# Kernel tuning notes

Hardware: AMD Instinct MI355X
Metric: run time of the kernel (lower is better)

The kernel has to match this reference:

```python
import jax, jax.numpy as jnp
import numpy as np

D = 1024       # num_feature == heads*dim_head
NHEADS = 16
HD = 64
INNER = NHEADS * HD
FF = 2048      # hardcoded mlp_dim in CSGO_model
L = 4          # depth
NOUT = 26      # hardcoded number of InvDynamic heads
IDH = 512      # inverse_dynamic_dim
B = 64
T = 32         # horizon


def _ln(x, g=None, b=None, eps=1e-5):
    mu = jnp.mean(x, axis=-1, keepdims=True)
    var = jnp.mean((x - mu) ** 2, axis=-1, keepdims=True)
    y = (x - mu) * jax.lax.rsqrt(var + eps)
    if g is not None:
        y = y * g + b
    return y


def setup_inputs() -> dict:
    key = jax.random.key(0)
    ks = jax.random.split(key, 20)
    s = 0.02
    inp = {
        'x': jax.random.normal(ks[0], (B, T, D), jnp.float32),
        # transformer params, stacked over depth L
        'qkv_w': jax.random.normal(ks[1], (L, D, 3 * INNER), jnp.float32) * s,
        'out_w': jax.random.normal(ks[2], (L, INNER, D), jnp.float32) * s,
        'out_b': jnp.zeros((L, D), jnp.float32),
        'attn_ln_g': jnp.ones((L, D), jnp.float32),
        'attn_ln_b': jnp.zeros((L, D), jnp.float32),
        'ff_ln_g': jnp.ones((L, D), jnp.float32),
        'ff_ln_b': jnp.zeros((L, D), jnp.float32),
        'ff_w1': jax.random.normal(ks[3], (L, D, FF), jnp.float32) * s,
        'ff_b1': jnp.zeros((L, FF), jnp.float32),
        'ff_w2': jax.random.normal(ks[4], (L, FF, D), jnp.float32) * s,
        'ff_b2': jnp.zeros((L, D), jnp.float32),
        # 26 InvDynamic heads, stacked
        'head_w1': jax.random.normal(ks[5], (NOUT, 2 * D, IDH), jnp.float32) * s,
        'head_b1': jnp.zeros((NOUT, IDH), jnp.float32),
        'head_w2': jax.random.normal(ks[6], (NOUT, IDH, IDH), jnp.float32) * s,
        'head_b2': jnp.zeros((NOUT, IDH), jnp.float32),
        'head_w3': jax.random.normal(ks[7], (NOUT, IDH, 1), jnp.float32) * s,
        'head_b3': jnp.zeros((NOUT, 1), jnp.float32),
    }
    return inp


def _forward(x, qkv_w, out_w, out_b, attn_ln_g, attn_ln_b, ff_ln_g, ff_ln_b,
             ff_w1, ff_b1, ff_w2, ff_b2,
             head_w1, head_b1, head_w2, head_b2, head_w3, head_b3):
    scale = HD ** -0.5

    def block(h, p):
        (qw, ow, ob, ag, ab, fg, fb, w1, b1, w2, b2) = p
        # x = attn(prenorm_ln(mid_ln(x))) + x  (mid LayerNorm has no affine, eps=1e-6)
        y = _ln(h, eps=1e-6)
        y = _ln(y, ag, ab)
        qkv = y @ qw                               # [B,T,3*INNER]
        q, k, v = jnp.split(qkv, 3, axis=-1)
        def split_heads(t):
            return t.reshape(t.shape[0], t.shape[1], NHEADS, HD).transpose(0, 2, 1, 3)
        q, k, v = split_heads(q), split_heads(k), split_heads(v)
        attn = jax.nn.softmax(jnp.einsum('bhqd,bhkd->bhqk', q, k) * scale, axis=-1)
        o = jnp.einsum('bhqk,bhkd->bhqd', attn, v)
        o = o.transpose(0, 2, 1, 3).reshape(h.shape[0], h.shape[1], INNER)
        h = h + (o @ ow + ob)
        # x = ff(prenorm_ln(x)) + x
        y = _ln(h, fg, fb)
        y = jax.nn.gelu(y @ w1 + b1, approximate=False) @ w2 + b2
        return h + y, None

    params = (qkv_w, out_w, out_b, attn_ln_g, attn_ln_b, ff_ln_g, ff_ln_b,
              ff_w1, ff_b1, ff_w2, ff_b2)
    x, _ = jax.lax.scan(block, x, params)

    # x_comb = concat(x[:,0], x[:,1])  -> [B, 2D]
    x_comb = jnp.concatenate([x[:, 0, :], x[:, 1, :]], axis=1)
    # 26 independent 3-layer MLP heads, batched as grouped GEMMs
    h1 = jax.nn.relu(jnp.einsum('bd,ndk->bnk', x_comb, head_w1) + head_b1)
    h2 = jax.nn.relu(jnp.einsum('bnk,nkj->bnj', h1, head_w2) + head_b2)
    out = jnp.einsum('bnk,nkj->bnj', h2, head_w3) + head_b3   # [B,26,1]
    return out


def reference(x, qkv_w, out_w, out_b, attn_ln_g, attn_ln_b, ff_ln_g, ff_ln_b,
              ff_w1, ff_b1, ff_w2, ff_b2,
              head_w1, head_b1, head_w2, head_b2, head_w3, head_b3):
    return _forward(x, qkv_w, out_w, out_b, attn_ln_g, attn_ln_b, ff_ln_g,
                    ff_ln_b, ff_w1, ff_b1, ff_w2, ff_b2,
                    head_w1, head_b1, head_w2, head_b2, head_w3, head_b3)
```

## Files before the change

### kernel.cpp

```cpp
#include <hip/hip_runtime.h>
#include <math.h>

static constexpr int BATCH = 64;
static constexpr int SEQ   = 32;
static constexpr int TOK   = BATCH * SEQ;
static constexpr int DIM   = 1024;
static constexpr int NH    = 16;
static constexpr int HDIM  = 64;
static constexpr int FFD   = 2048;
static constexpr int LAYERS= 4;
static constexpr int NHEAD_OUT = 26;
static constexpr int IDH   = 512;

typedef __bf16 bf16_t;
typedef __bf16 bf16x4 __attribute__((ext_vector_type(4)));
typedef __bf16 bf16x8 __attribute__((ext_vector_type(8)));
typedef float  f32x4  __attribute__((ext_vector_type(4)));
typedef float  f32x16 __attribute__((ext_vector_type(16)));
typedef unsigned short us4 __attribute__((ext_vector_type(4)));
typedef unsigned short us8 __attribute__((ext_vector_type(8)));

__device__ __forceinline__ unsigned short f2bfu(float f) {
    return __builtin_bit_cast(unsigned short, (bf16_t)f);
}

__device__ __forceinline__ void gload_lds16(const void* gp, void* lp) {
    __builtin_amdgcn_global_load_lds(
        (const __attribute__((address_space(1))) unsigned int*)gp,
        (__attribute__((address_space(3))) unsigned int*)lp,
        16, 0, 0);
}

__device__ __forceinline__ float block_sum(float v, float* red) {
    #pragma unroll
    for (int off = 32; off > 0; off >>= 1) v += __shfl_down(v, off);
    int lane = threadIdx.x & 63;
    int w    = threadIdx.x >> 6;
    if (lane == 0) red[w] = v;
    __syncthreads();
    float t = red[0] + red[1] + red[2] + red[3];
    __syncthreads();
    return t;
}

template<bool PRE, bool F32IN>
__global__ __launch_bounds__(256) void ln_kernel(const void* __restrict__ xv,
                                                 const float* __restrict__ g,
                                                 const float* __restrict__ b,
                                                 bf16_t* __restrict__ y,
                                                 bf16_t* __restrict__ hout) {
    __shared__ float red[4];
    long row = blockIdx.x;
    int tid = threadIdx.x;
    float4 v;
    if (F32IN) {
        const float* xr = (const float*)xv + row * DIM;
        v = *(const float4*)(xr + tid * 4);
        us4 hc;
        hc.x = f2bfu(v.x); hc.y = f2bfu(v.y); hc.z = f2bfu(v.z); hc.w = f2bfu(v.w);
        *(us4*)(hout + row * DIM + tid * 4) = hc;
        v.x = (float)(bf16_t)v.x; v.y = (float)(bf16_t)v.y;
        v.z = (float)(bf16_t)v.z; v.w = (float)(bf16_t)v.w;
    } else {
        const bf16_t* xr = (const bf16_t*)xv + row * DIM;
        bf16x4 r4 = *(const bf16x4*)(xr + tid * 4);
        v.x = (float)r4[0]; v.y = (float)r4[1]; v.z = (float)r4[2]; v.w = (float)r4[3];
    }
    if (PRE) {
        float s  = block_sum(v.x + v.y + v.z + v.w, red);
        float mu = s * (1.0f / DIM);
        v.x -= mu; v.y -= mu; v.z -= mu; v.w -= mu;
        float ss = block_sum(v.x*v.x + v.y*v.y + v.z*v.z + v.w*v.w, red);
        float r  = 1.0f / sqrtf(ss * (1.0f / DIM) + 1e-6f);
        v.x *= r; v.y *= r; v.z *= r; v.w *= r;
    }
    float s  = block_sum(v.x + v.y + v.z + v.w, red);
    float mu = s * (1.0f / DIM);
    v.x -= mu; v.y -= mu; v.z -= mu; v.w -= mu;
    float ss = block_sum(v.x*v.x + v.y*v.y + v.z*v.z + v.w*v.w, red);
    float r  = 1.0f / sqrtf(ss * (1.0f / DIM) + 1e-5f);
    float4 gg = *(const float4*)(g + tid * 4);
    float4 bb = *(const float4*)(b + tid * 4);
    us4 o;
    o.x = f2bfu(v.x * r * gg.x + bb.x);
    o.y = f2bfu(v.y * r * gg.y + bb.y);
    o.z = f2bfu(v.z * r * gg.z + bb.z);
    o.w = f2bfu(v.w * r * gg.w + bb.w);
    *(us4*)(y + row * DIM + tid * 4) = o;
}

struct TxPack {
    const float* src[4];
    bf16_t*      dst[4];
    int K[4], N[4];
    int blk0[4];
};

__global__ __launch_bounds__(256) void txd(TxPack p) {
    int bid = blockIdx.x;
    int s = 0;
    #pragma unroll
    for (int i = 1; i < 4; ++i) if (bid >= p.blk0[i]) s = i;
    int base = (bid - p.blk0[s]) * 4;
    int K = p.K[s], N = p.N[s];
    int nkb = K >> 6;
    int cpg = (N >> 5) * nkb;
    int kk = threadIdx.x >> 6;
    int l  = threadIdx.x & 63;
    int nl = l & 31, k8 = (l >> 5) * 8;
    #pragma unroll
    for (int qq = 0; qq < 2; ++qq) {
        int c0 = base + qq * 2, c1 = c0 + 1;
        int g0 = c0 / cpg, r0 = c0 - g0 * cpg;
        int g1 = c1 / cpg, r1 = c1 - g1 * cpg;
        int ns0 = r0 / nkb, kt0 = r0 - ns0 * nkb;
        int ns1 = r1 / nkb, kt1 = r1 - ns1 * nkb;
        const float* s0 = p.src[s] + (long)g0 * K * N
                        + (long)(kt0 * 64 + kk * 16 + k8) * N + ns0 * 32 + nl;
        const float* s1 = p.src[s] + (long)g1 * K * N
                        + (long)(kt1 * 64 + kk * 16 + k8) * N + ns1 * 32 + nl;
        float av[8], bv[8];
        #pragma unroll
        for (int j = 0; j < 8; ++j) av[j] = s0[(long)j * N];
        #pragma unroll
        for (int j = 0; j < 8; ++j) bv[j] = s1[(long)j * N];
        us8 oa, ob2;
        #pragma unroll
        for (int j = 0; j < 8; ++j) { oa[j] = f2bfu(av[j]); ob2[j] = f2bfu(bv[j]); }
        *(us8*)(p.dst[s] + (long)c0 * 2048 + kk * 512 + l * 8) = oa;
        *(us8*)(p.dst[s] + (long)c1 * 2048 + kk * 512 + l * 8) = ob2;
    }
}

template<int BM, int BN, int WM, int WN, int EPI>
__global__ __launch_bounds__(256) void gemm32(
    const bf16_t* __restrict__ A, const bf16_t* __restrict__ BT,
    const float* __restrict__ bias, const bf16_t* __restrict__ resid,
    bf16_t* __restrict__ Ch,
    int M, int N, int K)
{
    constexpr int WAVES_N = BN / WN;
    constexpr int FM = WM / 32, FN = WN / 32;
    constexpr int NSTG = BM / 32 + BN / 32;

    __shared__ bf16_t As[2][BM * 64];
    __shared__ bf16_t Bs[2][BN * 64];

    int tid  = threadIdx.x;
    int wave = tid >> 6, lane = tid & 63;
    int wr = wave / WAVES_N, wc = wave % WAVES_N;
    int m0 = blockIdx.y * BM, n0 = blockIdx.x * BN;

    f32x16 acc[FM][FN];
    #pragma unroll
    for (int m = 0; m < FM; ++m)
        #pragma unroll
        for (int n = 0; n < FN; ++n)
            #pragma unroll
            for (int r = 0; r < 16; ++r)
                acc[m][n][r] = 0.f;

    long rsb = (long)K * 2;
    int  lr  = lane & 31;
    int  lkb = (lane >> 5) * 16;
    int  nkb = K >> 6;

    const char* Abase = (const char*)A + (long)(m0 + lr) * rsb + lkb;
    const char* Bbase = (const char*)BT + (long)(n0 >> 5) * nkb * 4096 + lane * 16;

    auto stage = [&](int c, int t) {
        long kb = (long)t * 128;
        #pragma unroll
        for (int i = 0; i < BM / 32; ++i) {
            int b = i * 4 + wave;
            gload_lds16(Abase + (long)(b >> 2) * 32 * rsb + (b & 3) * 32 + kb,
                        (char*)&As[c][0] + b * 1024);
        }
        #pragma unroll
        for (int i = 0; i < BN / 32; ++i) {
            int b = i * 4 + wave;
            gload_lds16(Bbase + ((long)(b >> 2) * nkb + t) * 4096 + (b & 3) * 1024,
                        (char*)&Bs[c][0] + b * 1024);
        }
    };

    int nt = K >> 6;
    stage(0, 0);
    int cur = 0;
    for (int t = 0; t < nt; ++t) {
        if (t + 1 < nt) {
            stage(cur ^ 1, t + 1);
            asm volatile("s_waitcnt vmcnt(%c0)" :: "i"(NSTG) : "memory");
        } else {
            asm volatile("s_waitcnt vmcnt(0)" ::: "memory");
        }
        __builtin_amdgcn_s_barrier();
        asm volatile("" ::: "memory");
        bf16x8 af[FM][4], bq[FN][4];
        #pragma unroll
        for (int m = 0; m < FM; ++m)
            #pragma unroll
            for (int kk = 0; kk < 4; ++kk)
                af[m][kk] = *(const bf16x8*)((const char*)&As[cur][0] +
                            ((wr * FM + m) * 4 + kk) * 1024 + (lane << 4));
        #pragma unroll
        for (int n = 0; n < FN; ++n)
            #pragma unroll
            for (int kk = 0; kk < 4; ++kk)
                bq[n][kk] = *(const bf16x8*)((const char*)&Bs[cur][0] +
                            ((wc * FN + n) * 4 + kk) * 1024 + (lane << 4));
        #pragma unroll
        for (int kk = 0; kk < 4; ++kk)
            #pragma unroll
            for (int m = 0; m < FM; ++m)
                #pragma unroll
                for (int n = 0; n < FN; ++n)
                    acc[m][n] = __builtin_amdgcn_mfma_f32_32x32x16_bf16(
                        af[m][kk], bq[n][kk], acc[m][n], 0, 0, 0);
        asm volatile("" ::: "memory");
        __builtin_amdgcn_s_barrier();
        cur ^= 1;
    }

    int rbase = 4 * (lane >> 5);
    #pragma unroll
    for (int m = 0; m < FM; ++m) {
        #pragma unroll
        for (int n = 0; n < FN; ++n) {
            int colI = n0 + wc * WN + n * 32 + (lane & 31);
            float bb = (EPI != 0) ? bias[colI] : 0.f;
            #pragma unroll
            for (int r = 0; r < 16; ++r) {
                int rowI = m0 + wr * WM + m * 32 + rbase + (r & 3) + 8 * (r >> 2);
                float v = acc[m][n][r] + bb;
                if (EPI == 2) v = 0.5f * v * (1.0f + erff(v * 0.70710678118654752f));
                long off = (long)rowI * N + colI;
                if (EPI == 1) v += (float)resid[off];
                Ch[off] = (bf16_t)v;
            }
        }
    }
}

__global__ __launch_bounds__(256) void gemm_hd(
    const bf16_t* __restrict__ A, const float* __restrict__ Bw,
    const float* __restrict__ bias, bf16_t* __restrict__ C,
    int N, int K, long aStride, long sA, long sB, long sbias, long sC)
{
    long g = blockIdx.z;
    A += g * sA;
    const float* Bp = Bw + g * sB;
    bias += g * sbias;
    bf16_t* Cp = C + g * sC;

    __shared__ bf16_t As[2][64 * 64];
    __shared__ float  Bf[2][64 * 64];

    int tid = threadIdx.x, wave = tid >> 6, lane = tid & 63;
    int wr = wave >> 1, wc = wave & 1;
    int n0 = blockIdx.x * 64;

    f32x4 acc[2][2];
    #pragma unroll
    for (int m = 0; m < 2; ++m)
        #pragma unroll
        for (int n = 0; n < 2; ++n)
            acc[m][n] = f32x4{0.f, 0.f, 0.f, 0.f};

    long rsb = aStride * 2;
    int  lr  = lane & 15;
    int  lkb = (lane >> 4) * 16;
    const char* Abase = (const char*)A + (long)lr * rsb + lkb;

    auto stage = [&](int c, int t) {
        long kb = (long)t * 128;
        #pragma unroll
        for (int i = 0; i < 2; ++i) {
            int b = i * 4 + wave;
            gload_lds16(Abase + (long)(b >> 1) * 16 * rsb + (b & 1) * 64 + kb,
                        (char*)&As[c][0] + b * 1024);
        }
        #pragma unroll
        for (int i = 0; i < 4; ++i) {
            int ch = i * 4 + wave;
            int row = ch * 4 + (lane >> 4);
            gload_lds16((const char*)Bp + ((long)(t * 64 + row) * N + n0) * 4 + (lane & 15) * 16,
                        (char*)&Bf[c][0] + ch * 1024);
        }
    };

    int nt = K >> 6;
    stage(0, 0);
    int cur = 0;
    for (int t = 0; t < nt; ++t) {
        if (t + 1 < nt) {
            stage(cur ^ 1, t + 1);
            asm volatile("s_waitcnt vmcnt(6)" ::: "memory");
        } else {
            asm volatile("s_waitcnt vmcnt(0)" ::: "memory");
        }
        __builtin_amdgcn_s_barrier();
        asm volatile("" ::: "memory");
        bf16x8 af[2][2], bq[2][2];
        #pragma unroll
        for (int m = 0; m < 2; ++m)
            #pragma unroll
            for (int h = 0; h < 2; ++h)
                af[m][h] = *(const bf16x8*)((const char*)&As[cur][0] +
                           ((wr * 2 + m) * 2 + h) * 1024 + (lane << 4));
        #pragma unroll
        for (int n = 0; n < 2; ++n) {
            int nl = wc * 32 + n * 16 + lr;
            #pragma unroll
            for (int h = 0; h < 2; ++h) {
                #pragma unroll
                for (int j = 0; j < 8; ++j) {
                    float v = Bf[cur][(h * 32 + (lane >> 4) * 8 + j) * 64 + nl];
                    bq[n][h][j] = (bf16_t)v;
                }
            }
        }
        #pragma unroll
        for (int h = 0; h < 2; ++h)
            #pragma unroll
            for (int m = 0; m < 2; ++m)
                #pragma unroll
                for (int n = 0; n < 2; ++n)
                    acc[m][n] = __builtin_amdgcn_mfma_f32_16x16x32_bf16(
                        af[m][h], bq[n][h], acc[m][n], 0, 0, 0);
        asm volatile("" ::: "memory");
        __builtin_amdgcn_s_barrier();
        cur ^= 1;
    }

    int lq = (lane >> 4) * 4;
    #pragma unroll
    for (int m = 0; m < 2; ++m) {
        #pragma unroll
        for (int n = 0; n < 2; ++n) {
            int colI = n0 + wc * 32 + n * 16 + lr;
            float bb = bias[colI];
            #pragma unroll
            for (int j = 0; j < 4; ++j) {
                int rowI = wr * 32 + m * 16 + lq + j;
                float v = fmaxf(acc[m][n][j] + bb, 0.0f);
                Cp[(long)rowI * N + colI] = (bf16_t)v;
            }
        }
    }
}

__global__ __launch_bounds__(256) void attn_kernel(const bf16_t* __restrict__ qkv,
                                                   bf16_t* __restrict__ o) {
    int bh = blockIdx.x;
    int b  = bh >> 4;
    int hh = bh & 15;
    __shared__ float qs[32][65];
    __shared__ float kt[64][36];
    __shared__ float vs[32][68];
    __shared__ float ps[32][33];
    const bf16_t* base = qkv + (long)b * SEQ * (3 * DIM) + hh * HDIM;
    int tid = threadIdx.x;

    {
        int t = tid >> 3, c = (tid & 7) * 8;
        bf16x8 qv = *(const bf16x8*)(base + (long)t * 3 * DIM + c);
        bf16x8 kv = *(const bf16x8*)(base + (long)t * 3 * DIM + DIM + c);
        bf16x8 vv = *(const bf16x8*)(base + (long)t * 3 * DIM + 2 * DIM + c);
        #pragma unroll
        for (int j = 0; j < 8; ++j) {
            int d = c + j;
            qs[t][d] = (float)qv[j];
            kt[d][(((t >> 2) ^ ((d >> 2) & 7)) << 2) + (t & 3)] = (float)kv[j];
            vs[t][d] = (float)vv[j];
        }
    }
    __syncthreads();

    {
        int r  = tid >> 3;
        int c0 = (tid & 7) * 4;
        f32x4 acc = {0.f, 0.f, 0.f, 0.f};
        #pragma unroll
        for (int d = 0; d < 64; ++d) {
            float qv = qs[r][d];
            float4 kv = *(const float4*)&kt[d][(((c0 >> 2) ^ ((d >> 2) & 7)) << 2)];
            acc[0] = fmaf(qv, kv.x, acc[0]);
            acc[1] = fmaf(qv, kv.y, acc[1]);
            acc[2] = fmaf(qv, kv.z, acc[2]);
            acc[3] = fmaf(qv, kv.w, acc[3]);
        }
        #pragma unroll
        for (int i = 0; i < 4; ++i) ps[r][c0 + i] = acc[i] * 0.125f;
    }
    __syncthreads();

    if (tid < 32) {
        float mx = -1e30f;
        for (int c = 0; c < 32; ++c) mx = fmaxf(mx, ps[tid][c]);
        float sum = 0.f;
        for (int c = 0; c < 32; ++c) { float e = expf(ps[tid][c] - mx); ps[tid][c] = e; sum += e; }
        float inv = 1.f / sum;
        for (int c = 0; c < 32; ++c) ps[tid][c] *= inv;
    }
    __syncthreads();

    {
        int r  = tid >> 3;
        int d0 = (tid & 7) * 8;
        float acc[8] = {};
        #pragma unroll
        for (int c = 0; c < 32; ++c) {
            float pv = ps[r][c];
            float4 v0 = *(const float4*)&vs[c][d0];
            float4 v1 = *(const float4*)&vs[c][d0 + 4];
            acc[0] = fmaf(pv, v0.x, acc[0]);
            acc[1] = fmaf(pv, v0.y, acc[1]);
            acc[2] = fmaf(pv, v0.z, acc[2]);
            acc[3] = fmaf(pv, v0.w, acc[3]);
            acc[4] = fmaf(pv, v1.x, acc[4]);
            acc[5] = fmaf(pv, v1.y, acc[5]);
            acc[6] = fmaf(pv, v1.z, acc[6]);
            acc[7] = fmaf(pv, v1.w, acc[7]);
        }
        us8 ov;
        #pragma unroll
        for (int j = 0; j < 8; ++j) ov[j] = f2bfu(acc[j]);
        *(us8*)(o + (long)b * SEQ * DIM + (long)r * DIM + hh * HDIM + d0) = ov;
    }
}

__global__ __launch_bounds__(256) void head3_kernel(const bf16_t* __restrict__ h2,
                                                    const float* __restrict__ w3,
                                                    const float* __restrict__ b3,
                                                    float* __restrict__ out) {
    int gid  = blockIdx.x * 256 + threadIdx.x;
    int wave = gid >> 6;
    int lane = gid & 63;
    if (wave >= NHEAD_OUT * BATCH) return;
    int n = wave >> 6;
    int b = wave & 63;
    const bf16_t* a = h2 + ((long)n * BATCH + b) * IDH;
    const float*  w = w3 + (long)n * IDH;
    float acc = 0.f;
    #pragma unroll
    for (int i = lane; i < IDH; i += 64) acc = fmaf((float)a[i], w[i], acc);
    #pragma unroll
    for (int off = 32; off > 0; off >>= 1) acc += __shfl_down(acc, off);
    if (lane == 0) out[b * NHEAD_OUT + n] = acc + b3[n];
}

extern "C" void kernel_launch(void* const* d_in, const int* in_sizes, int n_in,
                              void* d_out, int out_size, void* d_ws, size_t ws_size,
                              hipStream_t stream) {
    const float* x      = (const float*)d_in[0];
    const float* qkv_w  = (const float*)d_in[1];
    const float* out_w  = (const float*)d_in[2];
    const float* out_b  = (const float*)d_in[3];
    const float* attn_g = (const float*)d_in[4];
    const float* attn_b = (const float*)d_in[5];
    const float* ff_g   = (const float*)d_in[6];
    const float* ff_b   = (const float*)d_in[7];
    const float* ff_w1  = (const float*)d_in[8];
    const float* ff_b1  = (const float*)d_in[9];
    const float* ff_w2  = (const float*)d_in[10];
    const float* ff_b2  = (const float*)d_in[11];
    const float* hw1    = (const float*)d_in[12];
    const float* hb1    = (const float*)d_in[13];
    const float* hw2    = (const float*)d_in[14];
    const float* hb2    = (const float*)d_in[15];
    const float* hw3    = (const float*)d_in[16];
    const float* hb3    = (const float*)d_in[17];
    float* out = (float*)d_out;

    char* p = (char*)d_ws;
    bf16_t* h     = (bf16_t*)p;           p += (long)TOK * DIM * 2;
    bf16_t* qkvb  = (bf16_t*)p;           p += (long)TOK * 3 * DIM * 2;
    bf16_t* y     = (bf16_t*)p;           p += (long)TOK * DIM * 2;
    bf16_t* ob    = (bf16_t*)p;           p += (long)TOK * DIM * 2;
    bf16_t* ffb   = (bf16_t*)p;           p += (long)TOK * FFD * 2;
    bf16_t* h1    = (bf16_t*)p;           p += (long)NHEAD_OUT * BATCH * IDH * 2;
    bf16_t* h2    = (bf16_t*)p;           p += (long)NHEAD_OUT * BATCH * IDH * 2;
    bf16_t* qkvwt = (bf16_t*)p;           p += (long)LAYERS * DIM * 3 * DIM * 2;
    bf16_t* outwt = (bf16_t*)p;           p += (long)LAYERS * DIM * DIM * 2;
    bf16_t* ff1t  = (bf16_t*)p;           p += (long)LAYERS * DIM * FFD * 2;
    bf16_t* ff2t  = (bf16_t*)p;           p += (long)LAYERS * FFD * DIM * 2;

    TxPack tp;
    tp.src[0] = qkv_w; tp.dst[0] = qkvwt; tp.K[0] = DIM; tp.N[0] = 3 * DIM;
    tp.src[1] = out_w; tp.dst[1] = outwt; tp.K[1] = DIM; tp.N[1] = DIM;
    tp.src[2] = ff_w1; tp.dst[2] = ff1t;  tp.K[2] = DIM; tp.N[2] = FFD;
    tp.src[3] = ff_w2; tp.dst[3] = ff2t;  tp.K[3] = FFD; tp.N[3] = DIM;
    int nblk = 0;
    for (int i = 0; i < 4; ++i) {
        tp.blk0[i] = nblk;
        nblk += LAYERS * (tp.N[i] >> 5) * (tp.K[i] >> 6) / 4;
    }
    txd<<<nblk, 256, 0, stream>>>(tp);

    for (int l = 0; l < LAYERS; ++l) {
        if (l == 0)
            ln_kernel<true, true><<<TOK, 256, 0, stream>>>(
                x, attn_g, attn_b, y, h);
        else
            ln_kernel<true, false><<<TOK, 256, 0, stream>>>(
                h, attn_g + l * DIM, attn_b + l * DIM, y, nullptr);
        gemm32<64, 128, 32, 64, 0><<<dim3(3 * DIM / 128, TOK / 64), 256, 0, stream>>>(
            y, qkvwt + (long)l * DIM * 3 * DIM, nullptr, nullptr, qkvb,
            TOK, 3 * DIM, DIM);
        attn_kernel<<<BATCH * NH, 256, 0, stream>>>(qkvb, ob);
        gemm32<64, 64, 32, 32, 1><<<dim3(DIM / 64, TOK / 64), 256, 0, stream>>>(
            ob, outwt + (long)l * DIM * DIM, out_b + l * DIM, h, h,
            TOK, DIM, DIM);
        ln_kernel<false, false><<<TOK, 256, 0, stream>>>(
            h, ff_g + l * DIM, ff_b + l * DIM, y, nullptr);
        gemm32<64, 128, 32, 64, 2><<<dim3(FFD / 128, TOK / 64), 256, 0, stream>>>(
            y, ff1t + (long)l * DIM * FFD, ff_b1 + l * FFD, nullptr, ffb,
            TOK, FFD, DIM);
        gemm32<64, 64, 32, 32, 1><<<dim3(DIM / 64, TOK / 64), 256, 0, stream>>>(
            ffb, ff2t + (long)l * FFD * DIM, ff_b2 + l * DIM, h, h,
            TOK, DIM, FFD);
    }

    gemm_hd<<<dim3(IDH / 64, 1, NHEAD_OUT), 256, 0, stream>>>(
        h, hw1, hb1, h1,
        IDH, 2 * DIM, (long)SEQ * DIM,
        0, (long)2 * DIM * IDH, IDH, (long)BATCH * IDH);
    gemm_hd<<<dim3(IDH / 64, 1, NHEAD_OUT), 256, 0, stream>>>(
        h1, hw2, hb2, h2,
        IDH, IDH, IDH,
        (long)BATCH * IDH, (long)IDH * IDH, IDH, (long)BATCH * IDH);
    head3_kernel<<<(NHEAD_OUT * BATCH * 64) / 256, 256, 0, stream>>>(h2, hw3, hb3, out);
}
```

Before: 526.5 us.

## Overlap next-layer weight conversion with current-layer GEMMs via extra blocks

```diff
diff --git a/kernel.cpp b/kernel.cpp
--- a/kernel.cpp
+++ b/kernel.cpp
@@ -29,6 +29,44 @@
         (const __attribute__((address_space(1))) unsigned int*)gp,
         (__attribute__((address_space(3))) unsigned int*)lp,
         16, 0, 0);
+}
+
+__device__ __forceinline__ void tx_chunks4(const float* __restrict__ src,
+                                           bf16_t* __restrict__ dst,
+                                           int K, int N, int base4) {
+    int nkb = K >> 6;
+    int kk = threadIdx.x >> 6;
+    int l  = threadIdx.x & 63;
+    int nl = l & 31, k8 = (l >> 5) * 8;
+    int base = base4 * 4;
+    #pragma unroll
+    for (int q = 0; q < 4; ++q) {
+        int chunk = base + q;
+        int ns = chunk / nkb;
+        int kt = chunk - ns * nkb;
+        int n = ns * 32 + nl;
+        int kb = kt * 64 + kk * 16 + k8;
+        us8 o;
+        #pragma unroll
+        for (int j = 0; j < 8; ++j)
+            o[j] = f2bfu(src[(long)(kb + j) * N + n]);
+        *(us8*)(dst + (long)chunk * 2048 + kk * 512 + l * 8) = o;
+    }
+}
+
+struct TxPack {
+    const float* src[4];
+    bf16_t*      dst[4];
+    int K[4], N[4];
+    int blk0[4];
+};
+
+__global__ __launch_bounds__(256) void txd(TxPack p) {
+    int bid = blockIdx.x;
+    int s = 0;
+    #pragma unroll
+    for (int i = 1; i < 4; ++i) if (bid >= p.blk0[i]) s = i;
+    tx_chunks4(p.src[s], p.dst[s], p.K[s], p.N[s], bid - p.blk0[s]);
 }
 
 __device__ __forceinline__ float block_sum(float v, float* red) {
@@ -89,55 +127,14 @@
     *(us4*)(y + row * DIM + tid * 4) = o;
 }
 
-struct TxPack {
-    const float* src[4];
-    bf16_t*      dst[4];
-    int K[4], N[4];
-    int blk0[4];
-};
-
-__global__ __launch_bounds__(256) void txd(TxPack p) {
-    int bid = blockIdx.x;
-    int s = 0;
-    #pragma unroll
-    for (int i = 1; i < 4; ++i) if (bid >= p.blk0[i]) s = i;
-    int base = (bid - p.blk0[s]) * 4;
-    int K = p.K[s], N = p.N[s];
-    int nkb = K >> 6;
-    int cpg = (N >> 5) * nkb;
-    int kk = threadIdx.x >> 6;
-    int l  = threadIdx.x & 63;
-    int nl = l & 31, k8 = (l >> 5) * 8;
-    #pragma unroll
-    for (int qq = 0; qq < 2; ++qq) {
-        int c0 = base + qq * 2, c1 = c0 + 1;
-        int g0 = c0 / cpg, r0 = c0 - g0 * cpg;
-        int g1 = c1 / cpg, r1 = c1 - g1 * cpg;
-        int ns0 = r0 / nkb, kt0 = r0 - ns0 * nkb;
-        int ns1 = r1 / nkb, kt1 = r1 - ns1 * nkb;
-        const float* s0 = p.src[s] + (long)g0 * K * N
-                        + (long)(kt0 * 64 + kk * 16 + k8) * N + ns0 * 32 + nl;
-        const float* s1 = p.src[s] + (long)g1 * K * N
-                        + (long)(kt1 * 64 + kk * 16 + k8) * N + ns1 * 32 + nl;
-        float av[8], bv[8];
-        #pragma unroll
-        for (int j = 0; j < 8; ++j) av[j] = s0[(long)j * N];
-        #pragma unroll
-        for (int j = 0; j < 8; ++j) bv[j] = s1[(long)j * N];
-        us8 oa, ob2;
-        #pragma unroll
-        for (int j = 0; j < 8; ++j) { oa[j] = f2bfu(av[j]); ob2[j] = f2bfu(bv[j]); }
-        *(us8*)(p.dst[s] + (long)c0 * 2048 + kk * 512 + l * 8) = oa;
-        *(us8*)(p.dst[s] + (long)c1 * 2048 + kk * 512 + l * 8) = ob2;
-    }
-}
-
 template<int BM, int BN, int WM, int WN, int EPI>
 __global__ __launch_bounds__(256) void gemm32(
     const bf16_t* __restrict__ A, const bf16_t* __restrict__ BT,
     const float* __restrict__ bias, const bf16_t* __restrict__ resid,
     bf16_t* __restrict__ Ch,
-    int M, int N, int K)
+    int N, int K, int gemmBlocks, int gx,
+    const float* __restrict__ txsrc, bf16_t* __restrict__ txdst,
+    int txK, int txN)
 {
     constexpr int WAVES_N = BN / WN;
     constexpr int FM = WM / 32, FN = WN / 32;
@@ -146,10 +143,17 @@
     __shared__ bf16_t As[2][BM * 64];
     __shared__ bf16_t Bs[2][BN * 64];
 
+    int bid = blockIdx.x;
+    if (bid >= gemmBlocks) {
+        tx_chunks4(txsrc, txdst, txK, txN, bid - gemmBlocks);
+        return;
+    }
+    int bx = bid % gx, by = bid / gx;
+
     int tid  = threadIdx.x;
     int wave = tid >> 6, lane = tid & 63;
     int wr = wave / WAVES_N, wc = wave % WAVES_N;
-    int m0 = blockIdx.y * BM, n0 = blockIdx.x * BN;
+    int m0 = by * BM, n0 = bx * BN;
 
     f32x16 acc[FM][FN];
     #pragma unroll
@@ -486,40 +490,66 @@
     bf16_t* ff1t  = (bf16_t*)p;           p += (long)LAYERS * DIM * FFD * 2;
     bf16_t* ff2t  = (bf16_t*)p;           p += (long)LAYERS * FFD * DIM * 2;
 
+    const long sQ = (long)DIM * 3 * DIM;
+    const long sO = (long)DIM * DIM;
+    const long sF1 = (long)DIM * FFD;
+    const long sF2 = (long)FFD * DIM;
+    const int tbQ  = (3 * DIM / 32) * (DIM / 64) / 4;
+    const int tbO  = (DIM / 32) * (DIM / 64) / 4;
+    const int tbF1 = (FFD / 32) * (DIM / 64) / 4;
+    const int tbF2 = (DIM / 32) * (FFD / 64) / 4;
+
     TxPack tp;
     tp.src[0] = qkv_w; tp.dst[0] = qkvwt; tp.K[0] = DIM; tp.N[0] = 3 * DIM;
     tp.src[1] = out_w; tp.dst[1] = outwt; tp.K[1] = DIM; tp.N[1] = DIM;
     tp.src[2] = ff_w1; tp.dst[2] = ff1t;  tp.K[2] = DIM; tp.N[2] = FFD;
     tp.src[3] = ff_w2; tp.dst[3] = ff2t;  tp.K[3] = FFD; tp.N[3] = DIM;
-    int nblk = 0;
-    for (int i = 0; i < 4; ++i) {
-        tp.blk0[i] = nblk;
-        nblk += LAYERS * (tp.N[i] >> 5) * (tp.K[i] >> 6) / 4;
-    }
-    txd<<<nblk, 256, 0, stream>>>(tp);
+    tp.blk0[0] = 0;
+    tp.blk0[1] = tbQ;
+    tp.blk0[2] = tbQ + tbO;
+    tp.blk0[3] = tbQ + tbO + tbF1;
+    txd<<<tbQ + tbO + tbF1 + tbF2, 256, 0, stream>>>(tp);
 
     for (int l = 0; l < LAYERS; ++l) {
+        bool more = (l + 1 < LAYERS);
         if (l == 0)
             ln_kernel<true, true><<<TOK, 256, 0, stream>>>(
                 x, attn_g, attn_b, y, h);
         else
             ln_kernel<true, false><<<TOK, 256, 0, stream>>>(
                 h, attn_g + l * DIM, attn_b + l * DIM, y, nullptr);
-        gemm32<64, 128, 32, 64, 0><<<dim3(3 * DIM / 128, TOK / 64), 256, 0, stream>>>(
-            y, qkvwt + (long)l * DIM * 3 * DIM, nullptr, nullptr, qkvb,
-            TOK, 3 * DIM, DIM);
+
+        {
+            int gx = 3 * DIM / 128, gb = gx * (TOK / 64);
+            gemm32<64, 128, 32, 64, 0><<<gb + (more ? tbQ : 0), 256, 0, stream>>>(
+                y, qkvwt + l * sQ, nullptr, nullptr, qkvb,
+                3 * DIM, DIM, gb, gx,
+                qkv_w + (l + 1) * sQ, qkvwt + (l + 1) * sQ, DIM, 3 * DIM);
+        }
         attn_kernel<<<BATCH * NH, 256, 0, stream>>>(qkvb, ob);
-        gemm32<64, 64, 32, 32, 1><<<dim3(DIM / 64, TOK / 64), 256, 0, stream>>>(
-            ob, outwt + (long)l * DIM * DIM, out_b + l * DIM, h, h,
-            TOK, DIM, DIM);
+        {
+            int gx = DIM / 64, gb = gx * (TOK / 64);
+            gemm32<64, 64, 32, 32, 1><<<gb + (more ? tbO : 0), 256, 0, stream>>>(
+                ob, outwt + l * sO, out_b + l * DIM, h, h,
+                DIM, DIM, gb, gx,
+                out_w + (l + 1) * sO, outwt + (l + 1) * sO, DIM, DIM);
+        }
         ln_kernel<false, false><<<TOK, 256, 0, stream>>>(
             h, ff_g + l * DIM, ff_b + l * DIM, y, nullptr);
-        gemm32<64, 128, 32, 64, 2><<<dim3(FFD / 128, TOK / 64), 256, 0, stream>>>(
-            y, ff1t + (long)l * DIM * FFD, ff_b1 + l * FFD, nullptr, ffb,
-            TOK, FFD, DIM);
-        gemm32<64, 64, 32, 32, 1><<<dim3(DIM / 64, TOK / 64), 256, 0, stream>>>(
-            ffb, ff2t + (long)l * FFD * DIM, ff_b2 + l * DIM, h, h,
-            TOK, DIM, FFD);
+        {
+            int gx = FFD / 128, gb = gx * (TOK / 64);
+            gemm32<64, 128, 32, 64, 2><<<gb + (more ? tbF1 : 0), 256, 0, stream>>>(
+                y, ff1t + l * sF1, ff_b1 + l * FFD, nullptr, ffb,
+                FFD, DIM, gb, gx,
+                ff_w1 + (l + 1) * sF1, ff1t + (l + 1) * sF1, DIM, FFD);
+        }
+        {
+            int gx = DIM / 64, gb = gx * (TOK / 64);
+            gemm32<64, 64, 32, 32, 1><<<gb + (more ? tbF2 : 0), 256, 0, stream>>>(
+                ffb, ff2t + l * sF2, ff_b2 + l * DIM, h, h,
+                DIM, FFD, gb, gx,
+                ff_w2 + (l + 1) * sF2, ff2t + (l + 1) * sF2, FFD, DIM);
+        }
     }
 
     gemm_hd<<<dim3(IDH / 64, 1, NHEAD_OUT), 256, 0, stream>>>(
```

After: 518.6 us (median of 2 runs). About the same (-1.5%).
